# Optimization experiments

Measured on AMD Instinct MI355X. Metric: run time of the kernel, lower is better.

## Reference

```python
import jax, jax.numpy as jnp
import numpy as np

B, S, D, H = 4, 2048, 512, 8
HD = D // H  # head_dim = 64


def setup_inputs() -> dict:
    key = jax.random.key(0)
    ks = jax.random.split(key, 16)
    sd = 1.0 / np.sqrt(D)
    def lin(ka, kb):
        W = jax.random.uniform(ka, (D, D), jnp.float32, -sd, sd)
        b = jax.random.uniform(kb, (D,), jnp.float32, -sd, sd)
        return W, b
    Wq, bq = lin(ks[0], ks[1])
    Wk, bk = lin(ks[2], ks[3])
    Wv, bv = lin(ks[4], ks[5])
    Wo, bo = lin(ks[6], ks[7])
    Ws, bs = lin(ks[8], ks[9])
    Wsh, bsh = lin(ks[10], ks[11])
    mod1_feat = jax.random.normal(ks[12], (B, S, D), jnp.float32)
    mod2_feat = jax.random.normal(ks[13], (B, S, D), jnp.float32)
    return {"mod1_feat": mod1_feat, "mod2_feat": mod2_feat,
            "Wq": Wq, "bq": bq, "Wk": Wk, "bk": bk, "Wv": Wv, "bv": bv,
            "Wo": Wo, "bo": bo, "Ws": Ws, "bs": bs, "Wsh": Wsh, "bsh": bsh}


def _heads(x):
    # [B, S, D] -> [B, H, S, HD]
    b, s, _ = x.shape
    return x.reshape(b, s, H, HD).transpose(0, 2, 1, 3)


def reference(mod1_feat, mod2_feat, Wq, bq, Wk, bk, Wv, bv, Wo, bo, Ws, bs, Wsh, bsh):
    Q = _heads(mod1_feat @ Wq + bq)
    K = _heads(mod2_feat @ Wk + bk)
    V = _heads(mod2_feat @ Wv + bv)
    scale = _heads(mod2_feat @ Ws + bs)
    shift = _heads(mod2_feat @ Wsh + bsh)
    K = K * scale + shift
    V = V * scale + shift
    scores = jnp.einsum('bhqd,bhkd->bhqk', Q, K) / jnp.sqrt(jnp.float32(HD))
    attn = jax.nn.softmax(scores, axis=-1)
    out = jnp.einsum('bhqk,bhkd->bhqd', attn, V)  # [B, H, S, HD]
    out = out.transpose(0, 2, 1, 3).reshape(mod1_feat.shape[0], -1, H * HD)
    return out @ Wo + bo
```

## Files before the change

### kernel.cpp

```cpp
#include <hip/hip_runtime.h>
#include <hip/hip_bf16.h>
#include <cstdint>
#include <cstddef>

typedef __bf16 bf16_t;
typedef __bf16 bf16x8 __attribute__((ext_vector_type(8)));
typedef __bf16 bf16x4 __attribute__((ext_vector_type(4)));
typedef float f32x4 __attribute__((ext_vector_type(4)));

#define DEVINL static __device__ __forceinline__

constexpr int B_ = 4, S_ = 2048, D_ = 512, H_ = 8, HD_ = 64;
constexpr int M_ = B_ * S_;
constexpr int NIN = 14;

DEVINL bf16x8 load8g(const bf16_t* p) { return *reinterpret_cast<const bf16x8*>(p); }

DEVINL int swcol(int col, int row) {
  return (col & ~63) | ((((col >> 3) ^ row) & 7) << 3) | (col & 7);
}

DEVINL int pK(int row) { return (row & 3) | (((row >> 3) & 1) << 2); }
DEVINL int swcolK(int col, int row) {
  return (col & ~63) | ((((col >> 3) ^ pK(row)) & 7) << 3) | (col & 7);
}

DEVINL void gl2lds(const bf16_t* g, bf16_t* l) {
  __builtin_amdgcn_global_load_lds(
      (const __attribute__((address_space(1))) void*)g,
      (__attribute__((address_space(3))) void*)l, 16, 0, 0);
}

DEVINL void stage16(bf16_t* dst, const void* src, size_t off, bool f32) {
  if (f32) {
    const float* p = (const float*)src + off;
    bf16x8 v0, v1;
#pragma unroll
    for (int j = 0; j < 8; ++j) { v0[j] = (bf16_t)p[j]; v1[j] = (bf16_t)p[8 + j]; }
    *reinterpret_cast<bf16x8*>(dst)     = v0;
    *reinterpret_cast<bf16x8*>(dst + 8) = v1;
  } else {
    const bf16_t* p = (const bf16_t*)src + off;
    *reinterpret_cast<bf16x8*>(dst)     = load8g(p);
    *reinterpret_cast<bf16x8*>(dst + 8) = load8g(p + 8);
  }
}

DEVINL float readf(const void* p, size_t i, bool f32) {
  return f32 ? ((const float*)p)[i] : (float)((const bf16_t*)p)[i];
}

struct DetectArgs { const uint16_t* p[NIN]; int n[NIN]; int* flags; };

__global__ __launch_bounds__(64) void detect_kernel(DetectArgs a) {
  const int z = blockIdx.x;
  const uint16_t* p = a.p[z];
  const int n = a.n[z];
  const int t = threadIdx.x;
  int cnt = 0;
  for (int i = t; i < n; i += 64) {
    const int e = (p[i] >> 7) & 0xFF;
    cnt += (e >= 200);
  }
#pragma unroll
  for (int off = 32; off > 0; off >>= 1) cnt += __shfl_down(cnt, off, 64);
  if (t == 0) a.flags[z] = (cnt > 16) ? 1 : 0;
}

struct CvtArgs { const void* src[2]; bf16_t* dst[2]; int idx[2]; const int* flags; };

__global__ __launch_bounds__(256) void cvt_kernel(CvtArgs a) {
  const int z = blockIdx.y;
  const bool f32 = a.flags[a.idx[z]] != 0;
  const size_t i = ((size_t)blockIdx.x * 256 + threadIdx.x) * 8;
  const int row = (int)(i >> 9);
  const int col = (int)(i & 511);
  bf16_t* dst = a.dst[z] + (size_t)row * 512 + swcol(col, row);
  if (f32) {
    const float* p = (const float*)a.src[z] + i;
    bf16x8 v;
#pragma unroll
    for (int j = 0; j < 8; ++j) v[j] = (bf16_t)p[j];
    *reinterpret_cast<bf16x8*>(dst) = v;
  } else {
    *reinterpret_cast<bf16x8*>(dst) = load8g((const bf16_t*)a.src[z] + i);
  }
}

struct TransArgs { const void* src[6]; int srcIdx[6]; bf16_t* dst[6]; const int* flags; };

__global__ __launch_bounds__(256) void transpose_kernel(TransArgs a) {
  __shared__ bf16_t tile[64][80];
  const int w = blockIdx.z;
  const void* src = a.src[w];
  const bool f32 = a.flags[a.srcIdx[w]] != 0;
  bf16_t* dst = a.dst[w];
  const int k0 = blockIdx.x * 64, n0 = blockIdx.y * 64;
  const int t = threadIdx.x;
  const int r = t >> 2, c0 = (t & 3) * 16;
  stage16(&tile[r][c0], src, (size_t)(k0 + r) * 512 + n0 + c0, f32);
  __syncthreads();
  const int orow = n0 + r;
  bf16_t* o = dst + (size_t)orow * 512;
#pragma unroll
  for (int half = 0; half < 2; ++half) {
    bf16x8 ov;
#pragma unroll
    for (int j = 0; j < 8; ++j) ov[j] = tile[c0 + half * 8 + j][r];
    *reinterpret_cast<bf16x8*>(o + swcol(k0 + c0 + half * 8, orow)) = ov;
  }
}

struct GemmBatch {
  const bf16_t* A[3];
  const bf16_t* Bt[3];
  const void* bias[3]; int bIdx[3];
  void* C[3];          int cIdx[3];
  const int* flags;
};

__global__ __launch_bounds__(256) void gemm_bt_kernel(GemmBatch args) {
  constexpr int K = 512, N = 512;
  __shared__ bf16_t As[2][128][64];
  __shared__ bf16_t Bs[2][64][64];
  const int z = blockIdx.z;
  const bf16_t* Ag  = args.A[z];
  const bf16_t* Btg = args.Bt[z];
  const void* biag  = args.bias[z];
  void* Cg          = args.C[z];
  const bool bf32 = args.bIdx[z] >= 0 && args.flags[args.bIdx[z]];
  const bool cf32 = args.cIdx[z] >= 0 && args.flags[args.cIdx[z]];
  const int m0 = blockIdx.x * 128, n0 = blockIdx.y * 64;
  const int t = threadIdx.x, lane = t & 63, wave = t >> 6;
  const int l16 = lane & 15, quad = lane >> 4;
  const int wm = wave * 32;
  const int lr = lane >> 3, lc = (lane & 7) * 8;

  auto stage = [&](int buf, int k0) {
#pragma unroll
    for (int s = 0; s < 4; ++s) {
      const int r = wm + s * 8;
      gl2lds(Ag + (size_t)(m0 + r + lr) * K + k0 + lc, &As[buf][r][0]);
    }
#pragma unroll
    for (int s = 0; s < 2; ++s) {
      const int r = wave * 16 + s * 8;
      gl2lds(Btg + (size_t)(n0 + r + lr) * K + k0 + lc, &Bs[buf][r][0]);
    }
  };

  f32x4 acc[2][4] = {};
  stage(0, 0);

  for (int kt = 0; kt < K / 64; ++kt) {
    const int cur = kt & 1;
    __syncthreads();
    if (kt + 1 < K / 64) stage(1 - cur, (kt + 1) * 64);
#pragma unroll
    for (int ks = 0; ks < 2; ++ks) {
      const int sw = swcol(ks * 32 + quad * 8, l16);
      bf16x8 af[2], bfr[4];
#pragma unroll
      for (int i = 0; i < 2; ++i)
        af[i] = *reinterpret_cast<const bf16x8*>(&As[cur][wm + i * 16 + l16][sw]);
#pragma unroll
      for (int j = 0; j < 4; ++j)
        bfr[j] = *reinterpret_cast<const bf16x8*>(&Bs[cur][j * 16 + l16][sw]);
#pragma unroll
      for (int i = 0; i < 2; ++i)
#pragma unroll
        for (int j = 0; j < 4; ++j)
          acc[i][j] = __builtin_amdgcn_mfma_f32_16x16x32_bf16(af[i], bfr[j], acc[i][j], 0, 0, 0);
    }
  }
#pragma unroll
  for (int j = 0; j < 4; ++j) {
    const int col = n0 + j * 16 + l16;
    const float bv = readf(biag, col, bf32);
#pragma unroll
    for (int i = 0; i < 2; ++i) {
      const int rowb = m0 + wm + i * 16 + quad * 4;
#pragma unroll
      for (int r = 0; r < 4; ++r) {
        const size_t idx = (size_t)(rowb + r) * N + col;
        const float v = acc[i][j][r] + bv;
        if (cf32) ((float*)Cg)[idx] = v;
        else      ((bf16_t*)Cg)[idx] = (bf16_t)v;
      }
    }
  }
}

struct GemmModArgs {
  const bf16_t* A;
  const bf16_t* Bt[2];
  const void* bias[2]; int bIdx[2];
  const bf16_t* Sc;
  const bf16_t* Sh;
  bf16_t* Kmod;
  bf16_t* VtT;
  const int* flags;
};

__global__ __launch_bounds__(256) void gemm_mod_kernel(GemmModArgs args) {
  constexpr int K = 512;
  __shared__ bf16_t As[2][128][64];
  __shared__ bf16_t Bs[2][64][64];
  const int z = blockIdx.z;
  const bf16_t* Ag  = args.A;
  const bf16_t* Btg = args.Bt[z];
  const void* biag  = args.bias[z];
  const bool bf32 = args.bIdx[z] >= 0 && args.flags[args.bIdx[z]];
  const int m0 = blockIdx.x * 128, n0 = blockIdx.y * 64;
  const int t = threadIdx.x, lane = t & 63, wave = t >> 6;
  const int l16 = lane & 15, quad = lane >> 4;
  const int wm = wave * 32;
  const int lr = lane >> 3, lc = (lane & 7) * 8;

  auto stage = [&](int buf, int k0) {
#pragma unroll
    for (int s = 0; s < 4; ++s) {
      const int r = wm + s * 8;
      gl2lds(Ag + (size_t)(m0 + r + lr) * K + k0 + lc, &As[buf][r][0]);
    }
#pragma unroll
    for (int s = 0; s < 2; ++s) {
      const int r = wave * 16 + s * 8;
      gl2lds(Btg + (size_t)(n0 + r + lr) * K + k0 + lc, &Bs[buf][r][0]);
    }
  };

  f32x4 acc[2][4] = {};
  stage(0, 0);

  for (int kt = 0; kt < K / 64; ++kt) {
    const int cur = kt & 1;
    __syncthreads();
    if (kt + 1 < K / 64) stage(1 - cur, (kt + 1) * 64);
#pragma unroll
    for (int ks = 0; ks < 2; ++ks) {
      const int sw = swcol(ks * 32 + quad * 8, l16);
      bf16x8 af[2], bfr[4];
#pragma unroll
      for (int i = 0; i < 2; ++i)
        af[i] = *reinterpret_cast<const bf16x8*>(&As[cur][wm + i * 16 + l16][sw]);
#pragma unroll
      for (int j = 0; j < 4; ++j)
        bfr[j] = *reinterpret_cast<const bf16x8*>(&Bs[cur][j * 16 + l16][sw]);
#pragma unroll
      for (int i = 0; i < 2; ++i)
#pragma unroll
        for (int j = 0; j < 4; ++j)
          acc[i][j] = __builtin_amdgcn_mfma_f32_16x16x32_bf16(af[i], bfr[j], acc[i][j], 0, 0, 0);
    }
  }
#pragma unroll
  for (int j = 0; j < 4; ++j) {
    const int col = n0 + j * 16 + l16;
    const float bv = readf(biag, col, bf32);
#pragma unroll
    for (int i = 0; i < 2; ++i) {
      const int rowb = m0 + wm + i * 16 + quad * 4;
      if (z == 0) {
#pragma unroll
        for (int r = 0; r < 4; ++r) {
          const int row = rowb + r;
          const size_t idx = (size_t)row * 512 + col;
          const float sc = (float)args.Sc[idx], sh = (float)args.Sh[idx];
          args.Kmod[(size_t)row * 512 + swcolK(col, row)] = (bf16_t)fmaf(acc[i][j][r] + bv, sc, sh);
        }
      } else {
        bf16x4 pack;
#pragma unroll
        for (int r = 0; r < 4; ++r) {
          const size_t idx = (size_t)(rowb + r) * 512 + col;
          const float sc = (float)args.Sc[idx], sh = (float)args.Sh[idx];
          pack[r] = (bf16_t)fmaf(acc[i][j][r] + bv, sc, sh);
        }
        const int bb = rowb >> 11;
        const int ss = rowb & 2047;
        const int hh = col >> 6, dd = col & 63;
        *reinterpret_cast<bf16x4*>(
            args.VtT + (((size_t)(bb * H_ + hh)) * HD_ + dd) * S_ + swcol(ss, dd)) = pack;
      }
    }
  }
}

__global__ __launch_bounds__(512) void attn_kernel(const bf16_t* Q, const bf16_t* Kb,
                                                   const bf16_t* Vt, bf16_t* O) {
  __shared__ bf16_t Ks[3][64][64];
  __shared__ bf16_t Vs[3][64][64];
  const int i = blockIdx.x;
  const int xcd = i & 7, g = i >> 3;
  const int slice = xcd * 4 + (g & 3);
  const int qt = g >> 2;
  const int b = slice >> 3, h = slice & 7;
  const int t = threadIdx.x, wave = t >> 6, lane = t & 63;
  const int l16 = lane & 15, quad = lane >> 4;
  const int q0 = qt * 128 + wave * 16;
  const int lr = lane >> 3, lc = (lane & 7) * 8;

  bf16x8 ones;
#pragma unroll
  for (int j = 0; j < 8; ++j) ones[j] = (bf16_t)1.0f;

  bf16x8 qf[2];
  {
    const size_t qrow = ((size_t)b * S_ + q0 + l16) * D_ + h * HD_;
    qf[0] = load8g(Q + qrow + quad * 8);
    qf[1] = load8g(Q + qrow + 32 + quad * 8);
  }

  f32x4 oacc[4] = {};
  f32x4 lacc = {};

  const size_t kbase = (size_t)b * S_ * D_ + h * HD_;
  const size_t vbase = ((size_t)(b * H_ + h)) * HD_ * S_;

  const int rbase = ((l16 >> 2) << 3) | (l16 & 3);
  int koff[2][4];
#pragma unroll
  for (int j = 0; j < 4; ++j) {
    const int rho = rbase + (j >> 1) * 32 + (j & 1) * 4;
#pragma unroll
    for (int dc = 0; dc < 2; ++dc)
      koff[dc][j] = rho * 64 + swcolK(dc * 32 + quad * 8, rho);
  }
  const int voff[2] = { swcol(quad * 8, l16), swcol(32 + quad * 8, l16) };

  auto stage = [&](int slot, int k0) {
    const int r = wave * 8;
    gl2lds(Kb + kbase + (size_t)(k0 + r + lr) * D_ + lc, &Ks[slot][r][0]);
    gl2lds(Vt + vbase + (size_t)(r + lr) * S_ + k0 + lc, &Vs[slot][r][0]);
  };

  constexpr float CE = 0.18033688011112042f;

  auto compute = [&](int cur) {
    f32x4 sacc[4] = {};
    const bf16_t* ksbase = &Ks[cur][0][0];
#pragma unroll
    for (int dc = 0; dc < 2; ++dc) {
      bf16x8 kf[4];
#pragma unroll
      for (int j = 0; j < 4; ++j)
        kf[j] = *reinterpret_cast<const bf16x8*>(ksbase + koff[dc][j]);
#pragma unroll
      for (int j = 0; j < 4; ++j)
        sacc[j] = __builtin_amdgcn_mfma_f32_16x16x32_bf16(kf[j], qf[dc], sacc[j], 0, 0, 0);
    }
#pragma unroll
    for (int kc = 0; kc < 2; ++kc) {
      bf16x8 vf[4];
#pragma unroll
      for (int dj = 0; dj < 4; ++dj)
        vf[dj] = *reinterpret_cast<const bf16x8*>(&Vs[cur][dj * 16 + l16][voff[kc]]);
      bf16x8 bp;
#pragma unroll
      for (int r = 0; r < 4; ++r) {
        bp[r]     = (bf16_t)__builtin_amdgcn_exp2f(fminf(sacc[kc * 2][r]     * CE, 57.5f));
        bp[4 + r] = (bf16_t)__builtin_amdgcn_exp2f(fminf(sacc[kc * 2 + 1][r] * CE, 57.5f));
      }
#pragma unroll
      for (int dj = 0; dj < 4; ++dj)
        oacc[dj] = __builtin_amdgcn_mfma_f32_16x16x32_bf16(vf[dj], bp, oacc[dj], 0, 0, 0);
      lacc = __builtin_amdgcn_mfma_f32_16x16x32_bf16(ones, bp, lacc, 0, 0, 0);
    }
  };

  stage(0, 0);
  stage(1, 64);

  constexpr int NT = S_ / 64;
  int cur = 0;
  for (int kt = 0; kt < NT - 1; ++kt) {
    asm volatile("s_waitcnt vmcnt(2)\n\ts_barrier" ::: "memory");
    __builtin_amdgcn_sched_barrier(0);
    if (kt + 2 < NT) {
      const int slot2 = cur == 0 ? 2 : cur - 1;
      stage(slot2, (kt + 2) * 64);
    }
    compute(cur);
    cur = (cur == 2) ? 0 : cur + 1;
  }
  asm volatile("s_waitcnt vmcnt(0)\n\ts_barrier" ::: "memory");
  __builtin_amdgcn_sched_barrier(0);
  compute(cur);

  {
    const float linv = 1.0f / fmaxf(lacc[0], 1e-30f);
    const int q = q0 + l16;
    const size_t orow = ((size_t)b * S_ + q) * D_ + h * HD_;
#pragma unroll
    for (int dj = 0; dj < 4; ++dj) {
      bf16x4 pack;
#pragma unroll
      for (int r = 0; r < 4; ++r) pack[r] = (bf16_t)(oacc[dj][r] * linv);
      *reinterpret_cast<bf16x4*>(&O[orow + swcol(dj * 16 + quad * 4, q)]) = pack;
    }
  }
}

extern "C" void kernel_launch(void* const* d_in, const int* in_sizes, int n_in,
                              void* d_out, int out_size, void* d_ws, size_t ws_size,
                              hipStream_t stream) {
  (void)n_in; (void)out_size; (void)ws_size;

  char* ws = (char*)d_ws;
  auto alloc = [&](size_t bytes) -> char* {
    char* p = ws; ws += (bytes + 255) & ~(size_t)255; return p;
  };
  int* flags = (int*)alloc(64 * sizeof(int));
  const size_t wbytes = (size_t)512 * 512 * sizeof(bf16_t);
  const size_t fbytes = (size_t)M_ * D_ * sizeof(bf16_t);
  bf16_t* wt    = (bf16_t*)alloc(6 * wbytes);
  bf16_t* m1b   = (bf16_t*)alloc(fbytes);
  bf16_t* m2b   = (bf16_t*)alloc(fbytes);
  bf16_t* q_buf = (bf16_t*)alloc(fbytes);
  bf16_t* stmp  = (bf16_t*)alloc(fbytes);
  bf16_t* shtmp = (bf16_t*)alloc(fbytes);
  bf16_t* kmod  = (bf16_t*)alloc(fbytes);
  bf16_t* vtb    = m1b;
  bf16_t* attn_b = stmp;

  bf16_t* wtq  = wt + 0 * 512 * 512;
  bf16_t* wtk  = wt + 1 * 512 * 512;
  bf16_t* wtv  = wt + 2 * 512 * 512;
  bf16_t* wts  = wt + 3 * 512 * 512;
  bf16_t* wtsh = wt + 4 * 512 * 512;
  bf16_t* wto  = wt + 5 * 512 * 512;

  DetectArgs da;
  for (int i = 0; i < NIN; ++i) {
    da.p[i] = (const uint16_t*)d_in[i];
    da.n[i] = in_sizes[i] < 2048 ? in_sizes[i] : 2048;
  }
  da.flags = flags;
  hipLaunchKernelGGL(detect_kernel, dim3(NIN), dim3(64), 0, stream, da);

  CvtArgs ca;
  ca.src[0] = d_in[0]; ca.dst[0] = m1b; ca.idx[0] = 0;
  ca.src[1] = d_in[1]; ca.dst[1] = m2b; ca.idx[1] = 1;
  ca.flags = flags;
  hipLaunchKernelGGL(cvt_kernel, dim3(M_ * D_ / 2048, 2), dim3(256), 0, stream, ca);

  TransArgs ta;
  const int widx[6] = {2, 4, 6, 10, 12, 8};
  bf16_t* wdst[6] = {wtq, wtk, wtv, wts, wtsh, wto};
  for (int i = 0; i < 6; ++i) { ta.src[i] = d_in[widx[i]]; ta.srcIdx[i] = widx[i]; ta.dst[i] = wdst[i]; }
  ta.flags = flags;
  hipLaunchKernelGGL(transpose_kernel, dim3(8, 8, 6), dim3(256), 0, stream, ta);

  GemmBatch g1;
  g1.A[0] = m1b; g1.A[1] = m2b; g1.A[2] = m2b;
  g1.Bt[0] = wtq; g1.Bt[1] = wts; g1.Bt[2] = wtsh;
  g1.bias[0] = d_in[3];  g1.bIdx[0] = 3;
  g1.bias[1] = d_in[11]; g1.bIdx[1] = 11;
  g1.bias[2] = d_in[13]; g1.bIdx[2] = 13;
  g1.C[0] = q_buf; g1.cIdx[0] = -1;
  g1.C[1] = stmp;  g1.cIdx[1] = -1;
  g1.C[2] = shtmp; g1.cIdx[2] = -1;
  g1.flags = flags;
  hipLaunchKernelGGL(gemm_bt_kernel, dim3(M_ / 128, 8, 3), dim3(256), 0, stream, g1);

  GemmModArgs gm;
  gm.A = m2b;
  gm.Bt[0] = wtk; gm.Bt[1] = wtv;
  gm.bias[0] = d_in[5]; gm.bIdx[0] = 5;
  gm.bias[1] = d_in[7]; gm.bIdx[1] = 7;
  gm.Sc = stmp; gm.Sh = shtmp;
  gm.Kmod = kmod; gm.VtT = vtb;
  gm.flags = flags;
  hipLaunchKernelGGL(gemm_mod_kernel, dim3(M_ / 128, 8, 2), dim3(256), 0, stream, gm);

  hipLaunchKernelGGL(attn_kernel, dim3(512), dim3(512), 0, stream,
                     q_buf, kmod, vtb, attn_b);

  GemmBatch g2;
  for (int i = 0; i < 3; ++i) {
    g2.A[i] = attn_b;
    g2.Bt[i] = wto;
    g2.bias[i] = d_in[9]; g2.bIdx[i] = 9;
    g2.C[i] = d_out; g2.cIdx[i] = 0;
  }
  g2.flags = flags;
  hipLaunchKernelGGL(gemm_bt_kernel, dim3(M_ / 128, 8, 1), dim3(256), 0, stream, g2);
}
```

Measured before the change: 214.1 us.

## Use 8-wave blocks and a triple-buffered async pipeline in projection GEMMs

The projection GEMM kernels go from 4 waves to 8 waves per block, so each wave computes a 16x64 tile instead of 32x64. The k-loop changes from a double-buffered __syncthreads scheme to a triple-buffered gl2lds prefetch two stages ahead, with explicit vmcnt waits and barriers, matching the attention kernel's pipeline. The aim is to hide global-to-LDS latency and raise wave-level parallelism. The cost is more LDS per block and less register-level reuse per wave, since each A fragment now feeds only 4 MFMAs. A vmcnt(0) wait is also added before the attention prologue.

```diff
diff --git a/kernel.cpp b/kernel.cpp
--- a/kernel.cpp
+++ b/kernel.cpp
@@ -119,74 +119,86 @@
   const int* flags;
 };
 
-__global__ __launch_bounds__(256) void gemm_bt_kernel(GemmBatch args) {
+__global__ __launch_bounds__(512) void gemm_bt_kernel(GemmBatch args) {
   constexpr int K = 512, N = 512;
-  __shared__ bf16_t As[2][128][64];
-  __shared__ bf16_t Bs[2][64][64];
+  __shared__ bf16_t As[3][128][64];
+  __shared__ bf16_t Bs[3][64][64];
   const int z = blockIdx.z;
   const bf16_t* Ag  = args.A[z];
   const bf16_t* Btg = args.Bt[z];
-  const void* biag  = args.bias[z];
-  void* Cg          = args.C[z];
-  const bool bf32 = args.bIdx[z] >= 0 && args.flags[args.bIdx[z]];
-  const bool cf32 = args.cIdx[z] >= 0 && args.flags[args.cIdx[z]];
   const int m0 = blockIdx.x * 128, n0 = blockIdx.y * 64;
   const int t = threadIdx.x, lane = t & 63, wave = t >> 6;
   const int l16 = lane & 15, quad = lane >> 4;
-  const int wm = wave * 32;
+  const int wm = wave * 16;
   const int lr = lane >> 3, lc = (lane & 7) * 8;
 
-  auto stage = [&](int buf, int k0) {
-#pragma unroll
-    for (int s = 0; s < 4; ++s) {
+  auto stage = [&](int slot, int k0) {
+#pragma unroll
+    for (int s = 0; s < 2; ++s) {
       const int r = wm + s * 8;
-      gl2lds(Ag + (size_t)(m0 + r + lr) * K + k0 + lc, &As[buf][r][0]);
-    }
-#pragma unroll
-    for (int s = 0; s < 2; ++s) {
-      const int r = wave * 16 + s * 8;
-      gl2lds(Btg + (size_t)(n0 + r + lr) * K + k0 + lc, &Bs[buf][r][0]);
-    }
+      gl2lds(Ag + (size_t)(m0 + r + lr) * K + k0 + lc, &As[slot][r][0]);
+    }
+    gl2lds(Btg + (size_t)(n0 + wave * 8 + lr) * K + k0 + lc, &Bs[slot][wave * 8][0]);
   };
 
-  f32x4 acc[2][4] = {};
+  f32x4 acc[4] = {};
+
   stage(0, 0);
-
-  for (int kt = 0; kt < K / 64; ++kt) {
-    const int cur = kt & 1;
-    __syncthreads();
-    if (kt + 1 < K / 64) stage(1 - cur, (kt + 1) * 64);
+  stage(1, 64);
+
+  constexpr int NT = K / 64;
+  int cur = 0;
+  for (int kt = 0; kt < NT - 1; ++kt) {
+    asm volatile("s_waitcnt vmcnt(3)\n\ts_barrier" ::: "memory");
+    __builtin_amdgcn_sched_barrier(0);
+    if (kt + 2 < NT) {
+      const int slot2 = cur == 0 ? 2 : cur - 1;
+      stage(slot2, (kt + 2) * 64);
+    }
 #pragma unroll
     for (int ks = 0; ks < 2; ++ks) {
       const int sw = swcol(ks * 32 + quad * 8, l16);
-      bf16x8 af[2], bfr[4];
-#pragma unroll
-      for (int i = 0; i < 2; ++i)
-        af[i] = *reinterpret_cast<const bf16x8*>(&As[cur][wm + i * 16 + l16][sw]);
+      bf16x8 af = *reinterpret_cast<const bf16x8*>(&As[cur][wm + l16][sw]);
+      bf16x8 bfr[4];
 #pragma unroll
       for (int j = 0; j < 4; ++j)
         bfr[j] = *reinterpret_cast<const bf16x8*>(&Bs[cur][j * 16 + l16][sw]);
 #pragma unroll
-      for (int i = 0; i < 2; ++i)
-#pragma unroll
-        for (int j = 0; j < 4; ++j)
-          acc[i][j] = __builtin_amdgcn_mfma_f32_16x16x32_bf16(af[i], bfr[j], acc[i][j], 0, 0, 0);
-    }
-  }
+      for (int j = 0; j < 4; ++j)
+        acc[j] = __builtin_amdgcn_mfma_f32_16x16x32_bf16(af, bfr[j], acc[j], 0, 0, 0);
+    }
+    cur = (cur == 2) ? 0 : cur + 1;
+  }
+  asm volatile("s_waitcnt vmcnt(0)\n\ts_barrier" ::: "memory");
+  __builtin_amdgcn_sched_barrier(0);
+#pragma unroll
+  for (int ks = 0; ks < 2; ++ks) {
+    const int sw = swcol(ks * 32 + quad * 8, l16);
+    bf16x8 af = *reinterpret_cast<const bf16x8*>(&As[cur][wm + l16][sw]);
+    bf16x8 bfr[4];
+#pragma unroll
+    for (int j = 0; j < 4; ++j)
+      bfr[j] = *reinterpret_cast<const bf16x8*>(&Bs[cur][j * 16 + l16][sw]);
+#pragma unroll
+    for (int j = 0; j < 4; ++j)
+      acc[j] = __builtin_amdgcn_mfma_f32_16x16x32_bf16(af, bfr[j], acc[j], 0, 0, 0);
+  }
+
+  const void* biag = args.bias[z];
+  void* Cg         = args.C[z];
+  const bool bf32 = args.bIdx[z] >= 0 && args.flags[args.bIdx[z]];
+  const bool cf32 = args.cIdx[z] >= 0 && args.flags[args.cIdx[z]];
 #pragma unroll
   for (int j = 0; j < 4; ++j) {
     const int col = n0 + j * 16 + l16;
     const float bv = readf(biag, col, bf32);
-#pragma unroll
-    for (int i = 0; i < 2; ++i) {
-      const int rowb = m0 + wm + i * 16 + quad * 4;
-#pragma unroll
-      for (int r = 0; r < 4; ++r) {
-        const size_t idx = (size_t)(rowb + r) * N + col;
-        const float v = acc[i][j][r] + bv;
-        if (cf32) ((float*)Cg)[idx] = v;
-        else      ((bf16_t*)Cg)[idx] = (bf16_t)v;
-      }
+    const int rowb = m0 + wm + quad * 4;
+#pragma unroll
+    for (int r = 0; r < 4; ++r) {
+      const size_t idx = (size_t)(rowb + r) * N + col;
+      const float v = acc[j][r] + bv;
+      if (cf32) ((float*)Cg)[idx] = v;
+      else      ((bf16_t*)Cg)[idx] = (bf16_t)v;
     }
   }
 }
@@ -202,87 +214,99 @@
   const int* flags;
 };
 
-__global__ __launch_bounds__(256) void gemm_mod_kernel(GemmModArgs args) {
+__global__ __launch_bounds__(512) void gemm_mod_kernel(GemmModArgs args) {
   constexpr int K = 512;
-  __shared__ bf16_t As[2][128][64];
-  __shared__ bf16_t Bs[2][64][64];
+  __shared__ bf16_t As[3][128][64];
+  __shared__ bf16_t Bs[3][64][64];
   const int z = blockIdx.z;
   const bf16_t* Ag  = args.A;
   const bf16_t* Btg = args.Bt[z];
-  const void* biag  = args.bias[z];
-  const bool bf32 = args.bIdx[z] >= 0 && args.flags[args.bIdx[z]];
   const int m0 = blockIdx.x * 128, n0 = blockIdx.y * 64;
   const int t = threadIdx.x, lane = t & 63, wave = t >> 6;
   const int l16 = lane & 15, quad = lane >> 4;
-  const int wm = wave * 32;
+  const int wm = wave * 16;
   const int lr = lane >> 3, lc = (lane & 7) * 8;
 
-  auto stage = [&](int buf, int k0) {
-#pragma unroll
-    for (int s = 0; s < 4; ++s) {
+  auto stage = [&](int slot, int k0) {
+#pragma unroll
+    for (int s = 0; s < 2; ++s) {
       const int r = wm + s * 8;
-      gl2lds(Ag + (size_t)(m0 + r + lr) * K + k0 + lc, &As[buf][r][0]);
-    }
-#pragma unroll
-    for (int s = 0; s < 2; ++s) {
-      const int r = wave * 16 + s * 8;
-      gl2lds(Btg + (size_t)(n0 + r + lr) * K + k0 + lc, &Bs[buf][r][0]);
-    }
+      gl2lds(Ag + (size_t)(m0 + r + lr) * K + k0 + lc, &As[slot][r][0]);
+    }
+    gl2lds(Btg + (size_t)(n0 + wave * 8 + lr) * K + k0 + lc, &Bs[slot][wave * 8][0]);
   };
 
-  f32x4 acc[2][4] = {};
+  f32x4 acc[4] = {};
+
   stage(0, 0);
-
-  for (int kt = 0; kt < K / 64; ++kt) {
-    const int cur = kt & 1;
-    __syncthreads();
-    if (kt + 1 < K / 64) stage(1 - cur, (kt + 1) * 64);
+  stage(1, 64);
+
+  constexpr int NT = K / 64;
+  int cur = 0;
+  for (int kt = 0; kt < NT - 1; ++kt) {
+    asm volatile("s_waitcnt vmcnt(3)\n\ts_barrier" ::: "memory");
+    __builtin_amdgcn_sched_barrier(0);
+    if (kt + 2 < NT) {
+      const int slot2 = cur == 0 ? 2 : cur - 1;
+      stage(slot2, (kt + 2) * 64);
+    }
 #pragma unroll
     for (int ks = 0; ks < 2; ++ks) {
       const int sw = swcol(ks * 32 + quad * 8, l16);
-      bf16x8 af[2], bfr[4];
-#pragma unroll
-      for (int i = 0; i < 2; ++i)
-        af[i] = *reinterpret_cast<const bf16x8*>(&As[cur][wm + i * 16 + l16][sw]);
+      bf16x8 af = *reinterpret_cast<const bf16x8*>(&As[cur][wm + l16][sw]);
+      bf16x8 bfr[4];
 #pragma unroll
       for (int j = 0; j < 4; ++j)
         bfr[j] = *reinterpret_cast<const bf16x8*>(&Bs[cur][j * 16 + l16][sw]);
 #pragma unroll
-      for (int i = 0; i < 2; ++i)
-#pragma unroll
-        for (int j = 0; j < 4; ++j)
-          acc[i][j] = __builtin_amdgcn_mfma_f32_16x16x32_bf16(af[i], bfr[j], acc[i][j], 0, 0, 0);
-    }
-  }
+      for (int j = 0; j < 4; ++j)
+        acc[j] = __builtin_amdgcn_mfma_f32_16x16x32_bf16(af, bfr[j], acc[j], 0, 0, 0);
+    }
+    cur = (cur == 2) ? 0 : cur + 1;
+  }
+  asm volatile("s_waitcnt vmcnt(0)\n\ts_barrier" ::: "memory");
+  __builtin_amdgcn_sched_barrier(0);
+#pragma unroll
+  for (int ks = 0; ks < 2; ++ks) {
+    const int sw = swcol(ks * 32 + quad * 8, l16);
+    bf16x8 af = *reinterpret_cast<const bf16x8*>(&As[cur][wm + l16][sw]);
+    bf16x8 bfr[4];
+#pragma unroll
+    for (int j = 0; j < 4; ++j)
+      bfr[j] = *reinterpret_cast<const bf16x8*>(&Bs[cur][j * 16 + l16][sw]);
+#pragma unroll
+    for (int j = 0; j < 4; ++j)
+      acc[j] = __builtin_amdgcn_mfma_f32_16x16x32_bf16(af, bfr[j], acc[j], 0, 0, 0);
+  }
+
+  const void* biag = args.bias[z];
+  const bool bf32 = args.bIdx[z] >= 0 && args.flags[args.bIdx[z]];
 #pragma unroll
   for (int j = 0; j < 4; ++j) {
     const int col = n0 + j * 16 + l16;
     const float bv = readf(biag, col, bf32);
-#pragma unroll
-    for (int i = 0; i < 2; ++i) {
-      const int rowb = m0 + wm + i * 16 + quad * 4;
-      if (z == 0) {
-#pragma unroll
-        for (int r = 0; r < 4; ++r) {
-          const int row = rowb + r;
-          const size_t idx = (size_t)row * 512 + col;
-          const float sc = (float)args.Sc[idx], sh = (float)args.Sh[idx];
-          args.Kmod[(size_t)row * 512 + swcolK(col, row)] = (bf16_t)fmaf(acc[i][j][r] + bv, sc, sh);
-        }
-      } else {
-        bf16x4 pack;
-#pragma unroll
-        for (int r = 0; r < 4; ++r) {
-          const size_t idx = (size_t)(rowb + r) * 512 + col;
-          const float sc = (float)args.Sc[idx], sh = (float)args.Sh[idx];
-          pack[r] = (bf16_t)fmaf(acc[i][j][r] + bv, sc, sh);
-        }
-        const int bb = rowb >> 11;
-        const int ss = rowb & 2047;
-        const int hh = col >> 6, dd = col & 63;
-        *reinterpret_cast<bf16x4*>(
-            args.VtT + (((size_t)(bb * H_ + hh)) * HD_ + dd) * S_ + swcol(ss, dd)) = pack;
+    const int rowb = m0 + wm + quad * 4;
+    if (z == 0) {
+#pragma unroll
+      for (int r = 0; r < 4; ++r) {
+        const int row = rowb + r;
+        const size_t idx = (size_t)row * 512 + col;
+        const float sc = (float)args.Sc[idx], sh = (float)args.Sh[idx];
+        args.Kmod[(size_t)row * 512 + swcolK(col, row)] = (bf16_t)fmaf(acc[j][r] + bv, sc, sh);
       }
+    } else {
+      bf16x4 pack;
+#pragma unroll
+      for (int r = 0; r < 4; ++r) {
+        const size_t idx = (size_t)(rowb + r) * 512 + col;
+        const float sc = (float)args.Sc[idx], sh = (float)args.Sh[idx];
+        pack[r] = (bf16_t)fmaf(acc[j][r] + bv, sc, sh);
+      }
+      const int bb = rowb >> 11;
+      const int ss = rowb & 2047;
+      const int hh = col >> 6, dd = col & 63;
+      *reinterpret_cast<bf16x4*>(
+          args.VtT + (((size_t)(bb * H_ + hh)) * HD_ + dd) * S_ + swcol(ss, dd)) = pack;
     }
   }
 }
@@ -369,6 +393,7 @@
     }
   };
 
+  asm volatile("s_waitcnt vmcnt(0)" ::: "memory");
   stage(0, 0);
   stage(1, 64);
 
@@ -462,7 +487,7 @@
   g1.C[1] = stmp;  g1.cIdx[1] = -1;
   g1.C[2] = shtmp; g1.cIdx[2] = -1;
   g1.flags = flags;
-  hipLaunchKernelGGL(gemm_bt_kernel, dim3(M_ / 128, 8, 3), dim3(256), 0, stream, g1);
+  hipLaunchKernelGGL(gemm_bt_kernel, dim3(M_ / 128, 8, 3), dim3(512), 0, stream, g1);
 
   GemmModArgs gm;
   gm.A = m2b;
@@ -472,7 +497,7 @@
   gm.Sc = stmp; gm.Sh = shtmp;
   gm.Kmod = kmod; gm.VtT = vtb;
   gm.flags = flags;
-  hipLaunchKernelGGL(gemm_mod_kernel, dim3(M_ / 128, 8, 2), dim3(256), 0, stream, gm);
+  hipLaunchKernelGGL(gemm_mod_kernel, dim3(M_ / 128, 8, 2), dim3(512), 0, stream, gm);
 
   hipLaunchKernelGGL(attn_kernel, dim3(512), dim3(512), 0, stream,
                      q_buf, kmod, vtb, attn_b);
@@ -485,5 +510,5 @@
     g2.C[i] = d_out; g2.cIdx[i] = 0;
   }
   g2.flags = flags;
-  hipLaunchKernelGGL(gemm_bt_kernel, dim3(M_ / 128, 8, 1), dim3(256), 0, stream, g2);
-}
+  hipLaunchKernelGGL(gemm_bt_kernel, dim3(M_ / 128, 8, 1), dim3(512), 0, stream, g2);
+}
```

New measurement: 215.3 us. About the same (+0.6%).
